# Kernel tuning notes

Measured on AMD Instinct MI355X. Metric: run time of the kernel, lower is better.

## Reference

```python
import jax, jax.numpy as jnp
import numpy as np

WEIGHT_BIT = 8
ACT_BIT = 8
EPS = 1e-8

def ste_round(v):
    # straight-through estimator round (matches torch ste_round in QAT)
    return v + jax.lax.stop_gradient(jnp.round(v) - v)

def setup_inputs() -> dict:
    key = jax.random.key(0)
    k1, k2, k3, k4 = jax.random.split(key, 4)
    B, D_IN, D_OUT = 8192, 4096, 4096
    x = jax.random.normal(k1, (B, D_IN), dtype=jnp.float32)
    act_scaling_factor = jax.random.uniform(k2, (1,), dtype=jnp.float32, minval=0.01, maxval=0.05)
    W = jax.random.normal(k3, (D_OUT, D_IN), dtype=jnp.float32) * 0.02
    b = jax.random.normal(k4, (D_OUT,), dtype=jnp.float32) * 0.02
    return {"x": x, "act_scaling_factor": act_scaling_factor, "W": W, "b": b}

def reference(x, act_scaling_factor, W, b):
    n_w = 2 ** (WEIGHT_BIT - 1) - 1  # 127
    # ---- QuantLinear: symmetric per-channel weight quantization ----
    w_absmax = jnp.maximum(jnp.abs(W.min(axis=1)), jnp.abs(W.max(axis=1)))  # [out]
    fc_sf = jnp.maximum(w_absmax, EPS) / n_w  # weight scaling factor, [out]
    w_int = jnp.clip(ste_round(W / fc_sf[:, None]), -n_w - 1, n_w)
    bias_sf = fc_sf * act_scaling_factor  # [out] (act_sf is scalar-shaped [1])
    b_int = ste_round(b / bias_sf)
    x_int = x / act_scaling_factor
    out = (jnp.matmul(x_int, w_int.T) + b_int) * bias_sf  # [B, out]
    # ---- ReLU ----
    out = jax.nn.relu(out)
    # ---- QuantAct, asymmetric per-tensor requantization ----
    levels = 2 ** ACT_BIT - 1  # 255
    x_min = jnp.minimum(out.min(), 0.0)
    x_max = jnp.maximum(out.max(), 0.0)
    act_sf_new = jnp.maximum(x_max - x_min, EPS) / levels  # scalar
    zp = jnp.round(-x_min / act_sf_new)
    x_q = jnp.clip(ste_round(out / act_sf_new) + zp, 0.0, float(levels))
    x_out = (x_q - zp) * act_sf_new
    return (x_out, fc_sf, jnp.reshape(act_sf_new, (1,)))
```

## Files before the change

kernel.cpp:

```cpp
#include <hip/hip_runtime.h>
#include <hip/hip_bf16.h>
#include <stdint.h>

#define B_DIM 8192
#define IN_DIM 4096
#define OUT_DIM 4096

typedef __attribute__((ext_vector_type(8))) short s16x8;
typedef __attribute__((ext_vector_type(4))) float f32x4;

__device__ __forceinline__ unsigned short f2bf_rn(float f) {
    unsigned int u = __float_as_uint(f);
    u = (u + 0x7FFFu + ((u >> 16) & 1u)) >> 16;
    return (unsigned short)u;
}

__device__ __forceinline__ void async16(unsigned short* l, const unsigned short* g) {
    __builtin_amdgcn_global_load_lds(
        (const __attribute__((address_space(1))) void*)g,
        (__attribute__((address_space(3))) void*)l, 16, 0, 0);
}

__global__ __launch_bounds__(256) void prep(
    const float* __restrict__ W, const float* __restrict__ b,
    const float* __restrict__ act_sf, const float* __restrict__ x,
    unsigned short* __restrict__ wq, unsigned short* __restrict__ xq,
    float* __restrict__ fc_sf_out, float* __restrict__ bb,
    float* __restrict__ gmax)
{
    __shared__ float red[4];
    int t = threadIdx.x;
    if (blockIdx.x < OUT_DIM) {
        int o = blockIdx.x;
        const float4* Wr = (const float4*)(W + (size_t)o * IN_DIM);
        float4 v[4];
        float amax = 0.f;
#pragma unroll
        for (int j = 0; j < 4; ++j) {
            v[j] = Wr[t + j * 256];
            amax = fmaxf(amax, fmaxf(fmaxf(fabsf(v[j].x), fabsf(v[j].y)),
                                     fmaxf(fabsf(v[j].z), fabsf(v[j].w))));
        }
#pragma unroll
        for (int off = 32; off > 0; off >>= 1)
            amax = fmaxf(amax, __shfl_down(amax, off, 64));
        if ((t & 63) == 0) red[t >> 6] = amax;
        __syncthreads();
        float wmax = fmaxf(fmaxf(red[0], red[1]), fmaxf(red[2], red[3]));
        float sf = fmaxf(wmax, 1e-8f) / 127.0f;

        unsigned short* wr = wq + (size_t)o * IN_DIM;
#pragma unroll
        for (int j = 0; j < 4; ++j) {
            ushort4 q;
            q.x = f2bf_rn(fminf(fmaxf(rintf(v[j].x / sf), -128.f), 127.f));
            q.y = f2bf_rn(fminf(fmaxf(rintf(v[j].y / sf), -128.f), 127.f));
            q.z = f2bf_rn(fminf(fmaxf(rintf(v[j].z / sf), -128.f), 127.f));
            q.w = f2bf_rn(fminf(fmaxf(rintf(v[j].w / sf), -128.f), 127.f));
            ((ushort4*)wr)[t + j * 256] = q;
        }
        if (t == 0) {
            fc_sf_out[o] = sf;
            float bsf = sf * act_sf[0];
            float bi = rintf(b[o] / bsf);
            bb[o] = bi * bsf;
            if (o == 0) gmax[0] = 0.f;
        }
    } else {
        size_t i = ((size_t)(blockIdx.x - OUT_DIM) * 256 + t) * 8;
#pragma unroll
        for (int j = 0; j < 2; ++j) {
            float4 v = *(const float4*)(x + i + j * 4);
            ushort4 q;
            q.x = f2bf_rn(v.x); q.y = f2bf_rn(v.y);
            q.z = f2bf_rn(v.z); q.w = f2bf_rn(v.w);
            *(ushort4*)(xq + i + j * 4) = q;
        }
    }
}

template <bool CB16>
__global__ __launch_bounds__(256) void gemm_bt(
    const unsigned short* __restrict__ A, const unsigned short* __restrict__ Bw,
    const float* __restrict__ fc_sf, const float* __restrict__ bb,
    void* __restrict__ Cout, float* __restrict__ gmax)
{
    __shared__ __align__(16) unsigned char smem[33296];
    unsigned short* sA = (unsigned short*)smem;
    unsigned short* sB = (unsigned short*)(smem + 16384);
    float* stage = (float*)smem;
    float* redm  = (float*)(smem + 33280);

    int t = threadIdx.x;
    int bn = blockIdx.x & 31;
    int bm = blockIdx.x >> 5;
    int lane = t & 63;
    int w = t >> 6;
    int quad = lane >> 4;
    int l16 = lane & 15;
    int m0 = bm * 128, n0 = bn * 128;
    int wm = (w & 1) * 64, wn = (w >> 1) * 64;

    int r0 = t >> 3;
    int gc = (t & 7) ^ (r0 & 7);
    const unsigned short* gA[4];
    const unsigned short* gB[4];
    unsigned short* lA[4];
    unsigned short* lB[4];
#pragma unroll
    for (int j = 0; j < 4; ++j) {
        gA[j] = A + (size_t)(m0 + j * 32 + r0) * IN_DIM + gc * 8;
        gB[j] = Bw + (size_t)(n0 + j * 32 + r0) * IN_DIM + gc * 8;
        lA[j] = sA + (j * 256 + t) * 8;
        lB[j] = sB + (j * 256 + t) * 8;
    }

    int swzl = l16 & 7;
    const unsigned short* pa[2];
    const unsigned short* pb[2];
#pragma unroll
    for (int h = 0; h < 2; ++h) {
        pa[h] = sA + (wm + l16) * 64 + ((4 * h + quad) ^ swzl) * 8;
        pb[h] = sB + (wn + l16) * 64 + ((4 * h + quad) ^ swzl) * 8;
    }

    f32x4 acc[4][4];
#pragma unroll
    for (int mi = 0; mi < 4; ++mi)
#pragma unroll
        for (int ni = 0; ni < 4; ++ni)
            acc[mi][ni] = (f32x4){0.f, 0.f, 0.f, 0.f};

    for (int kk = 0; kk < IN_DIM; kk += 64) {
        __syncthreads();
#pragma unroll
        for (int j = 0; j < 4; ++j) {
            async16(lA[j], gA[j] + kk);
            async16(lB[j], gB[j] + kk);
        }
        asm volatile("s_waitcnt vmcnt(0)" ::: "memory");
        __syncthreads();

#pragma unroll
        for (int h = 0; h < 2; ++h) {
            s16x8 af[4], bf[4];
#pragma unroll
            for (int i = 0; i < 4; ++i) af[i] = *(const s16x8*)(pa[h] + i * 16 * 64);
#pragma unroll
            for (int i = 0; i < 4; ++i) bf[i] = *(const s16x8*)(pb[h] + i * 16 * 64);
#pragma unroll
            for (int mi = 0; mi < 4; ++mi)
#pragma unroll
                for (int ni = 0; ni < 4; ++ni)
                    acc[mi][ni] = __builtin_amdgcn_mfma_f32_16x16x32_bf16(
                        af[mi], bf[ni], acc[mi][ni], 0, 0, 0);
        }
    }

    float sc[4], bv[4];
#pragma unroll
    for (int ni = 0; ni < 4; ++ni) {
        int col = n0 + wn + ni * 16 + l16;
        sc[ni] = fc_sf[col];
        bv[ni] = bb[col];
    }
    float tmax = 0.f;
#pragma unroll
    for (int mi = 0; mi < 4; ++mi)
#pragma unroll
        for (int ni = 0; ni < 4; ++ni)
#pragma unroll
            for (int r = 0; r < 4; ++r) {
                float vv = fmaxf(acc[mi][ni][r] * sc[ni] + bv[ni], 0.f);
                acc[mi][ni][r] = vv;
                tmax = fmaxf(tmax, vv);
            }
#pragma unroll
    for (int off = 32; off > 0; off >>= 1)
        tmax = fmaxf(tmax, __shfl_down(tmax, off, 64));
    if (lane == 0) redm[w] = tmax;

#pragma unroll
    for (int p = 0; p < 2; ++p) {
        __syncthreads();
        if ((w & 1) == p) {
#pragma unroll
            for (int mi = 0; mi < 4; ++mi)
#pragma unroll
                for (int ni = 0; ni < 4; ++ni)
#pragma unroll
                    for (int r = 0; r < 4; ++r) {
                        int lrow = mi * 16 + quad * 4 + r;
                        stage[lrow * 130 + wn + ni * 16 + l16] = acc[mi][ni][r];
                    }
        }
        __syncthreads();
        int row = t >> 2;
        int cc = (t & 3) * 32;
        const float* src = stage + row * 130 + cc;
        size_t gbase = (size_t)(m0 + p * 64 + row) * OUT_DIM + n0 + cc;
        if (CB16) {
            unsigned short* dst = (unsigned short*)Cout + gbase;
#pragma unroll
            for (int j = 0; j < 4; ++j) {
                float4 v0 = *(const float4*)(src + j * 8);
                float4 v1 = *(const float4*)(src + j * 8 + 4);
                s16x8 q;
                q[0] = (short)f2bf_rn(v0.x); q[1] = (short)f2bf_rn(v0.y);
                q[2] = (short)f2bf_rn(v0.z); q[3] = (short)f2bf_rn(v0.w);
                q[4] = (short)f2bf_rn(v1.x); q[5] = (short)f2bf_rn(v1.y);
                q[6] = (short)f2bf_rn(v1.z); q[7] = (short)f2bf_rn(v1.w);
                *(s16x8*)(dst + j * 8) = q;
            }
        } else {
            float* dst = (float*)Cout + gbase;
#pragma unroll
            for (int j = 0; j < 8; ++j)
                *(float4*)(dst + j * 4) = *(const float4*)(src + j * 4);
        }
    }
    if (t == 0) {
        float bmax = fmaxf(fmaxf(redm[0], redm[1]), fmaxf(redm[2], redm[3]));
        atomicMax((int*)gmax, __float_as_int(bmax));
    }
}

template <bool CB16>
__global__ __launch_bounds__(256) void requant(const void* __restrict__ Cin,
    float* __restrict__ out, const float* __restrict__ gmax,
    float* __restrict__ sf_out)
{
    float sf = fmaxf(gmax[0], 1e-8f) / 255.0f;
    size_t i = ((size_t)blockIdx.x * 256 + threadIdx.x) * 16;
    if (CB16) {
        const unsigned short* cq = (const unsigned short*)Cin + i;
#pragma unroll
        for (int j = 0; j < 4; ++j) {
            ushort4 q = *(const ushort4*)(cq + j * 4);
            float4 v;
            v.x = __uint_as_float((unsigned)q.x << 16);
            v.y = __uint_as_float((unsigned)q.y << 16);
            v.z = __uint_as_float((unsigned)q.z << 16);
            v.w = __uint_as_float((unsigned)q.w << 16);
            v.x = fminf(rintf(v.x / sf), 255.f) * sf;
            v.y = fminf(rintf(v.y / sf), 255.f) * sf;
            v.z = fminf(rintf(v.z / sf), 255.f) * sf;
            v.w = fminf(rintf(v.w / sf), 255.f) * sf;
            *(float4*)(out + i + j * 4) = v;
        }
    } else {
        float* C = out;
#pragma unroll
        for (int j = 0; j < 4; ++j) {
            float4 v = *(const float4*)(C + i + j * 4);
            v.x = fminf(rintf(v.x / sf), 255.f) * sf;
            v.y = fminf(rintf(v.y / sf), 255.f) * sf;
            v.z = fminf(rintf(v.z / sf), 255.f) * sf;
            v.w = fminf(rintf(v.w / sf), 255.f) * sf;
            *(float4*)(C + i + j * 4) = v;
        }
    }
    if (i == 0) sf_out[0] = sf;
}

extern "C" void kernel_launch(void* const* d_in, const int* in_sizes, int n_in,
                              void* d_out, int out_size, void* d_ws, size_t ws_size,
                              hipStream_t stream)
{
    const float* x      = (const float*)d_in[0];
    const float* act_sf = (const float*)d_in[1];
    const float* W      = (const float*)d_in[2];
    const float* b      = (const float*)d_in[3];

    float* out        = (float*)d_out;
    float* fc_sf_out  = out + (size_t)B_DIM * OUT_DIM;
    float* act_sf_out = fc_sf_out + OUT_DIM;

    char* ws = (char*)d_ws;
    float* bb   = (float*)ws;
    float* gmax = (float*)(ws + 16384);
    unsigned short* xq = (unsigned short*)(ws + 32768);
    unsigned short* wq = xq + (size_t)B_DIM * IN_DIM;
    unsigned short* cq = wq + (size_t)OUT_DIM * IN_DIM;

    size_t need = 32768 + ((size_t)B_DIM * IN_DIM + (size_t)OUT_DIM * IN_DIM
                           + (size_t)B_DIM * OUT_DIM) * 2;

    prep<<<OUT_DIM + (B_DIM * IN_DIM) / 2048, 256, 0, stream>>>(
        W, b, act_sf, x, wq, xq, fc_sf_out, bb, gmax);

    int gemm_grid = (B_DIM / 128) * (OUT_DIM / 128);
    int rq_grid = (B_DIM * OUT_DIM) / 4096;
    if (ws_size >= need) {
        gemm_bt<true><<<gemm_grid, 256, 0, stream>>>(
            xq, wq, fc_sf_out, bb, (void*)cq, gmax);
        requant<true><<<rq_grid, 256, 0, stream>>>(
            (const void*)cq, out, gmax, act_sf_out);
    } else {
        gemm_bt<false><<<gemm_grid, 256, 0, stream>>>(
            xq, wq, fc_sf_out, bb, (void*)out, gmax);
        requant<false><<<rq_grid, 256, 0, stream>>>(
            (const void*)out, out, gmax, act_sf_out);
    }
}
```

Baseline: 617.6 us.

## Restructure GEMM to 256x256 tiles with 8 waves and double-buffered async LDS pipeline

Replaces the 128x128, 4-wave GEMM with a 256x256 tile, 512-thread block. K-tiles are double-buffered in 128KB of LDS and global loads are interleaved across four MFMA quadrants, with explicit barriers, waitcnt and setprio. It also remaps block IDs to group tiles for L2 locality. The aim is to hide global-load latency, which the old single-buffer load/wait/compute loop exposed every iteration, and to raise arithmetic intensity per byte loaded. In exchange it carries higher register pressure and occupancy of one block per CU, and the hand-written vmcnt accounting has to be exactly right.

```diff
diff --git a/kernel.cpp b/kernel.cpp
--- a/kernel.cpp
+++ b/kernel.cpp
@@ -5,6 +5,7 @@
 #define B_DIM 8192
 #define IN_DIM 4096
 #define OUT_DIM 4096
+#define NT (IN_DIM / 64)
 
 typedef __attribute__((ext_vector_type(8))) short s16x8;
 typedef __attribute__((ext_vector_type(4))) float f32x4;
@@ -80,99 +81,173 @@
 }
 
 template <bool CB16>
-__global__ __launch_bounds__(256) void gemm_bt(
+__global__ __launch_bounds__(512) void gemm_bt(
     const unsigned short* __restrict__ A, const unsigned short* __restrict__ Bw,
     const float* __restrict__ fc_sf, const float* __restrict__ bb,
     void* __restrict__ Cout, float* __restrict__ gmax)
 {
-    __shared__ __align__(16) unsigned char smem[33296];
-    unsigned short* sA = (unsigned short*)smem;
-    unsigned short* sB = (unsigned short*)(smem + 16384);
+    __shared__ __align__(16) unsigned char smem[131072];
+    unsigned short* lds = (unsigned short*)smem;
     float* stage = (float*)smem;
-    float* redm  = (float*)(smem + 33280);
+    float* redm  = (float*)(smem + 131040);
 
     int t = threadIdx.x;
-    int bn = blockIdx.x & 31;
-    int bm = blockIdx.x >> 5;
-    int lane = t & 63;
-    int w = t >> 6;
-    int quad = lane >> 4;
-    int l16 = lane & 15;
-    int m0 = bm * 128, n0 = bn * 128;
-    int wm = (w & 1) * 64, wn = (w >> 1) * 64;
+    int bid = ((blockIdx.x & 7) << 6) | (blockIdx.x >> 3);
+    int bm = bid >> 4, bn = bid & 15;
+    int m0 = bm << 8, n0 = bn << 8;
+
+    int w = t >> 6, lane = t & 63;
+    int wm = w & 1, wn = w >> 1;
+    int quad = lane >> 4, l16 = lane & 15;
+    int swz = l16 & 7;
+
+    int co0 = (quad ^ swz) << 3;
+    int co1 = ((quad + 4) ^ swz) << 3;
+    int aOff = ((wm << 4) + l16) << 6;
+    int bOff = 32768 + (((wn << 4) + l16) << 6);
 
     int r0 = t >> 3;
-    int gc = (t & 7) ^ (r0 & 7);
-    const unsigned short* gA[4];
-    const unsigned short* gB[4];
-    unsigned short* lA[4];
-    unsigned short* lB[4];
-#pragma unroll
-    for (int j = 0; j < 4; ++j) {
-        gA[j] = A + (size_t)(m0 + j * 32 + r0) * IN_DIM + gc * 8;
-        gB[j] = Bw + (size_t)(n0 + j * 32 + r0) * IN_DIM + gc * 8;
-        lA[j] = sA + (j * 256 + t) * 8;
-        lB[j] = sB + (j * 256 + t) * 8;
-    }
-
-    int swzl = l16 & 7;
-    const unsigned short* pa[2];
-    const unsigned short* pb[2];
-#pragma unroll
-    for (int h = 0; h < 2; ++h) {
-        pa[h] = sA + (wm + l16) * 64 + ((4 * h + quad) ^ swzl) * 8;
-        pb[h] = sB + (wn + l16) * 64 + ((4 * h + quad) ^ swzl) * 8;
-    }
-
-    f32x4 acc[4][4];
-#pragma unroll
-    for (int mi = 0; mi < 4; ++mi)
-#pragma unroll
-        for (int ni = 0; ni < 4; ++ni)
-            acc[mi][ni] = (f32x4){0.f, 0.f, 0.f, 0.f};
-
-    for (int kk = 0; kk < IN_DIM; kk += 64) {
-        __syncthreads();
-#pragma unroll
-        for (int j = 0; j < 4; ++j) {
-            async16(lA[j], gA[j] + kk);
-            async16(lB[j], gB[j] + kk);
-        }
-        asm volatile("s_waitcnt vmcnt(0)" ::: "memory");
-        __syncthreads();
-
-#pragma unroll
-        for (int h = 0; h < 2; ++h) {
-            s16x8 af[4], bf[4];
-#pragma unroll
-            for (int i = 0; i < 4; ++i) af[i] = *(const s16x8*)(pa[h] + i * 16 * 64);
-#pragma unroll
-            for (int i = 0; i < 4; ++i) bf[i] = *(const s16x8*)(pb[h] + i * 16 * 64);
-#pragma unroll
-            for (int mi = 0; mi < 4; ++mi)
-#pragma unroll
-                for (int ni = 0; ni < 4; ++ni)
-                    acc[mi][ni] = __builtin_amdgcn_mfma_f32_16x16x32_bf16(
-                        af[mi], bf[ni], acc[mi][ni], 0, 0, 0);
-        }
+    int cs = ((t & 7) ^ (r0 & 7)) << 3;
+    const unsigned short* gA = A + (size_t)(m0 + r0) * IN_DIM + cs;
+    const unsigned short* gB = Bw + (size_t)(n0 + r0) * IN_DIM + cs;
+    unsigned short* ldsA = lds + t * 8;
+    unsigned short* ldsB = lds + 32768 + t * 8;
+
+    auto stageA = [&](int u, int hf) {
+        if (u < NT) {
+            const unsigned short* s = gA + (size_t)(hf * 128) * IN_DIM + u * 64;
+            unsigned short* d = ldsA + ((u & 1) << 14) + (hf << 13);
+            async16(d, s);
+            async16(d + 4096, s + (size_t)64 * IN_DIM);
+        }
+    };
+    auto stageB = [&](int u, int hf) {
+        if (u < NT) {
+            const unsigned short* s = gB + (size_t)(hf * 128) * IN_DIM + u * 64;
+            unsigned short* d = ldsB + ((u & 1) << 14) + (hf << 13);
+            async16(d, s);
+            async16(d + 4096, s + (size_t)64 * IN_DIM);
+        }
+    };
+
+    f32x4 acc[8][4];
+#pragma unroll
+    for (int mi = 0; mi < 8; ++mi)
+#pragma unroll
+        for (int nj = 0; nj < 4; ++nj)
+            acc[mi][nj] = (f32x4){0.f, 0.f, 0.f, 0.f};
+
+    s16x8 aLo[4][2], aHi[4][2], bF[2][2];
+
+    stageA(0, 0); stageA(0, 1); stageB(0, 0); stageB(0, 1);
+    stageA(1, 0); stageA(1, 1); stageB(1, 0);
+    asm volatile("s_waitcnt vmcnt(6)" ::: "memory");
+    __builtin_amdgcn_s_barrier();
+
+    for (int kt = 0; kt < NT; ++kt) {
+        int bufo = (kt & 1) << 14;
+        const unsigned short* la = lds + bufo + aOff;
+        const unsigned short* lb = lds + bufo + bOff;
+
+#pragma unroll
+        for (int mi = 0; mi < 4; ++mi) {
+            aLo[mi][0] = *(const s16x8*)(la + mi * 2048 + co0);
+            aLo[mi][1] = *(const s16x8*)(la + mi * 2048 + co1);
+        }
+#pragma unroll
+        for (int nj = 0; nj < 2; ++nj) {
+            bF[nj][0] = *(const s16x8*)(lb + nj * 4096 + co0);
+            bF[nj][1] = *(const s16x8*)(lb + nj * 4096 + co1);
+        }
+        stageB(kt + 1, 1);
+        __builtin_amdgcn_s_barrier();
+        asm volatile("s_waitcnt lgkmcnt(0)" ::: "memory");
+        __builtin_amdgcn_sched_barrier(0);
+        __builtin_amdgcn_s_setprio(1);
+#pragma unroll
+        for (int mi = 0; mi < 4; ++mi)
+#pragma unroll
+            for (int nj = 0; nj < 2; ++nj) {
+                acc[mi][nj] = __builtin_amdgcn_mfma_f32_16x16x32_bf16(aLo[mi][0], bF[nj][0], acc[mi][nj], 0, 0, 0);
+                acc[mi][nj] = __builtin_amdgcn_mfma_f32_16x16x32_bf16(aLo[mi][1], bF[nj][1], acc[mi][nj], 0, 0, 0);
+            }
+        __builtin_amdgcn_s_setprio(0);
+        __builtin_amdgcn_s_barrier();
+
+#pragma unroll
+        for (int mi = 0; mi < 4; ++mi) {
+            aHi[mi][0] = *(const s16x8*)(la + 8192 + mi * 2048 + co0);
+            aHi[mi][1] = *(const s16x8*)(la + 8192 + mi * 2048 + co1);
+        }
+        stageA(kt + 2, 0);
+        __builtin_amdgcn_s_barrier();
+        asm volatile("s_waitcnt lgkmcnt(0)" ::: "memory");
+        __builtin_amdgcn_sched_barrier(0);
+        __builtin_amdgcn_s_setprio(1);
+#pragma unroll
+        for (int mi = 0; mi < 4; ++mi)
+#pragma unroll
+            for (int nj = 0; nj < 2; ++nj) {
+                acc[4 + mi][nj] = __builtin_amdgcn_mfma_f32_16x16x32_bf16(aHi[mi][0], bF[nj][0], acc[4 + mi][nj], 0, 0, 0);
+                acc[4 + mi][nj] = __builtin_amdgcn_mfma_f32_16x16x32_bf16(aHi[mi][1], bF[nj][1], acc[4 + mi][nj], 0, 0, 0);
+            }
+        __builtin_amdgcn_s_setprio(0);
+        __builtin_amdgcn_s_barrier();
+
+#pragma unroll
+        for (int nj = 0; nj < 2; ++nj) {
+            bF[nj][0] = *(const s16x8*)(lb + 8192 + nj * 4096 + co0);
+            bF[nj][1] = *(const s16x8*)(lb + 8192 + nj * 4096 + co1);
+        }
+        stageA(kt + 2, 1);
+        __builtin_amdgcn_s_barrier();
+        asm volatile("s_waitcnt lgkmcnt(0)" ::: "memory");
+        __builtin_amdgcn_sched_barrier(0);
+        __builtin_amdgcn_s_setprio(1);
+#pragma unroll
+        for (int mi = 0; mi < 4; ++mi)
+#pragma unroll
+            for (int nj = 0; nj < 2; ++nj) {
+                acc[4 + mi][2 + nj] = __builtin_amdgcn_mfma_f32_16x16x32_bf16(aHi[mi][0], bF[nj][0], acc[4 + mi][2 + nj], 0, 0, 0);
+                acc[4 + mi][2 + nj] = __builtin_amdgcn_mfma_f32_16x16x32_bf16(aHi[mi][1], bF[nj][1], acc[4 + mi][2 + nj], 0, 0, 0);
+            }
+        __builtin_amdgcn_s_setprio(0);
+        __builtin_amdgcn_s_barrier();
+
+        stageB(kt + 2, 0);
+        __builtin_amdgcn_s_barrier();
+        __builtin_amdgcn_s_setprio(1);
+#pragma unroll
+        for (int mi = 0; mi < 4; ++mi)
+#pragma unroll
+            for (int nj = 0; nj < 2; ++nj) {
+                acc[mi][2 + nj] = __builtin_amdgcn_mfma_f32_16x16x32_bf16(aLo[mi][0], bF[nj][0], acc[mi][2 + nj], 0, 0, 0);
+                acc[mi][2 + nj] = __builtin_amdgcn_mfma_f32_16x16x32_bf16(aLo[mi][1], bF[nj][1], acc[mi][2 + nj], 0, 0, 0);
+            }
+        __builtin_amdgcn_s_setprio(0);
+        if (kt + 2 < NT)
+            asm volatile("s_waitcnt vmcnt(6)" ::: "memory");
+        else if (kt + 2 == NT)
+            asm volatile("s_waitcnt vmcnt(0)" ::: "memory");
+        __builtin_amdgcn_s_barrier();
     }
 
     float sc[4], bv[4];
 #pragma unroll
-    for (int ni = 0; ni < 4; ++ni) {
-        int col = n0 + wn + ni * 16 + l16;
-        sc[ni] = fc_sf[col];
-        bv[ni] = bb[col];
+    for (int nj = 0; nj < 4; ++nj) {
+        int col = n0 + (((nj << 2) + wn) << 4) + l16;
+        sc[nj] = fc_sf[col];
+        bv[nj] = bb[col];
     }
     float tmax = 0.f;
 #pragma unroll
-    for (int mi = 0; mi < 4; ++mi)
-#pragma unroll
-        for (int ni = 0; ni < 4; ++ni)
+    for (int mi = 0; mi < 8; ++mi)
+#pragma unroll
+        for (int nj = 0; nj < 4; ++nj)
 #pragma unroll
             for (int r = 0; r < 4; ++r) {
-                float vv = fmaxf(acc[mi][ni][r] * sc[ni] + bv[ni], 0.f);
-                acc[mi][ni][r] = vv;
+                float vv = fmaxf(acc[mi][nj][r] * sc[nj] + bv[nj], 0.f);
+                acc[mi][nj][r] = vv;
                 tmax = fmaxf(tmax, vv);
             }
 #pragma unroll
@@ -181,24 +256,23 @@
     if (lane == 0) redm[w] = tmax;
 
 #pragma unroll
-    for (int p = 0; p < 2; ++p) {
+    for (int ph = 0; ph < 4; ++ph) {
         __syncthreads();
-        if ((w & 1) == p) {
-#pragma unroll
-            for (int mi = 0; mi < 4; ++mi)
-#pragma unroll
-                for (int ni = 0; ni < 4; ++ni)
-#pragma unroll
-                    for (int r = 0; r < 4; ++r) {
-                        int lrow = mi * 16 + quad * 4 + r;
-                        stage[lrow * 130 + wn + ni * 16 + l16] = acc[mi][ni][r];
-                    }
+#pragma unroll
+        for (int ml = 0; ml < 2; ++ml) {
+            int lrow = (((ml << 1) + wm) << 4) + (quad << 2);
+#pragma unroll
+            for (int nj = 0; nj < 4; ++nj) {
+                int col = (((nj << 2) + wn) << 4) + l16;
+#pragma unroll
+                for (int r = 0; r < 4; ++r)
+                    stage[(lrow + r) * 260 + col] = acc[ph * 2 + ml][nj][r];
+            }
         }
         __syncthreads();
-        int row = t >> 2;
-        int cc = (t & 3) * 32;
-        const float* src = stage + row * 130 + cc;
-        size_t gbase = (size_t)(m0 + p * 64 + row) * OUT_DIM + n0 + cc;
+        int row = t >> 3, ch = t & 7;
+        const float* src = stage + row * 260 + ch * 32;
+        size_t gbase = (size_t)(m0 + ph * 64 + row) * OUT_DIM + n0 + ch * 32;
         if (CB16) {
             unsigned short* dst = (unsigned short*)Cout + gbase;
 #pragma unroll
@@ -220,7 +294,9 @@
         }
     }
     if (t == 0) {
-        float bmax = fmaxf(fmaxf(redm[0], redm[1]), fmaxf(redm[2], redm[3]));
+        float bmax = redm[0];
+#pragma unroll
+        for (int i = 1; i < 8; ++i) bmax = fmaxf(bmax, redm[i]);
         atomicMax((int*)gmax, __float_as_int(bmax));
     }
 }
@@ -289,15 +365,15 @@
     prep<<<OUT_DIM + (B_DIM * IN_DIM) / 2048, 256, 0, stream>>>(
         W, b, act_sf, x, wq, xq, fc_sf_out, bb, gmax);
 
-    int gemm_grid = (B_DIM / 128) * (OUT_DIM / 128);
+    int gemm_grid = (B_DIM / 256) * (OUT_DIM / 256);
     int rq_grid = (B_DIM * OUT_DIM) / 4096;
     if (ws_size >= need) {
-        gemm_bt<true><<<gemm_grid, 256, 0, stream>>>(
+        gemm_bt<true><<<gemm_grid, 512, 0, stream>>>(
             xq, wq, fc_sf_out, bb, (void*)cq, gmax);
         requant<true><<<rq_grid, 256, 0, stream>>>(
             (const void*)cq, out, gmax, act_sf_out);
     } else {
-        gemm_bt<false><<<gemm_grid, 256, 0, stream>>>(
+        gemm_bt<false><<<gemm_grid, 512, 0, stream>>>(
             xq, wq, fc_sf_out, bb, (void*)out, gmax);
         requant<false><<<rq_grid, 256, 0, stream>>>(
             (const void*)out, out, gmax, act_sf_out);
```

Result: faster. 528.8 us (-14.4%).
